# Performance work log

Hardware: AMD Instinct MI355X
Metric: run time of the kernel (lower is better)

The kernel has to match this reference:

```python
import jax, jax.numpy as jnp
import numpy as np

B, P, S, D, H, DFF, F, FIN = 16, 25, 1024, 128, 8, 512, 1, 4
SIGMA, OMEGA = 0.1, 0.5
DH = D // H


def setup_inputs() -> dict:
    key = jax.random.key(0)
    ks = jax.random.split(key, 16)
    s = lambda i, sh, sc=1.0: jax.random.normal(ks[i], sh, dtype=jnp.float32) * sc
    return dict(
        x=s(0, (B, P, D)),
        y=s(1, (B, FIN, 1)),
        K=s(2, (B, P, S, D), 0.02),
        V=s(3, (B, P, S, D), 0.02),
        w=jnp.ones((B, P, 1), jnp.float32) / P,
        I=jax.random.randint(ks[4], (B, P, S), 0, P, dtype=jnp.int32),
        Wq=s(5, (D, D), 0.05), Wk=s(6, (D, D), 0.05),
        Wv=s(7, (D, D), 0.05), Wo=s(8, (D, D), 0.05),
        W1=s(9, (D, DFF), 0.05), b1=jnp.zeros((DFF,), jnp.float32),
        W2=s(10, (DFF, D), 0.05), b2=jnp.zeros((D,), jnp.float32),
        Wout=s(11, (D, F), 0.05), bout=jnp.zeros((F,), jnp.float32),
        eps_k=s(12, (B, P, 1, D)), eps_v=s(13, (B, P, 1, D)), eps_z=s(14, (B, P, 1, D)),
        t=512,
    )


def reference(x, y, K, V, w, I, Wq, Wk, Wv, Wo, W1, b1, W2, b2, Wout, bout,
              eps_k, eps_v, eps_z, t):
    # ---- MultiHeadAttention_SMC: per-particle self-attention with reparam noise ----
    xq = x[:, :, None, :]                                   # (B,P,1,D)
    q = xq @ Wq                                             # (B,P,1,D)
    k = xq @ Wk + SIGMA * eps_k                             # noisy key particle
    v = xq @ Wv + SIGMA * eps_v                             # noisy value particle
    K = K.at[:, :, t, :].set(k[:, :, 0, :])                 # write current step into state
    V = V.at[:, :, t, :].set(v[:, :, 0, :])
    q_h = q.reshape(B, P, 1, H, DH)
    K_h = K.reshape(B, P, S, H, DH)
    V_h = V.reshape(B, P, S, H, DH)
    scores = jnp.einsum('bpqhd,bpshd->bphqs', q_h, K_h) / jnp.sqrt(jnp.float32(DH))
    valid = (jnp.arange(S) <= t)[None, None, None, None, :]  # attend to steps <= t
    scores = jnp.where(valid, scores, jnp.float32(-1e9))
    attn = jax.nn.softmax(scores, axis=-1)                  # (B,P,H,1,S)
    ctx = jnp.einsum('bphqs,bpshd->bpqhd', attn, V_h).reshape(B, P, 1, D)
    z = ctx @ Wo + SIGMA * eps_z                            # reparametrized attention output

    # ---- FFN + output layer (dropout is identity at inference) ----
    r_ = jax.nn.relu(z @ W1 + b1) @ W2 + b2                 # (B,P,1,D)
    pred = r_ @ Wout + bout                                 # (B,P,1,F)

    p_t = pred[:, :, 0, :]                                  # (B,P,F)
    y_sq = y[..., 0]                                        # (B,FIN)
    y_t = jnp.broadcast_to(y_sq[:, None, 0:1], (B, P, F))   # target_feature = 0
    mu = y_t - p_t                                          # (B,P,F)
    log_w_full = jnp.einsum('bpf,bqf->bpq', mu, mu) * (-0.5 * OMEGA)
    log_w = jnp.diagonal(log_w_full, axis1=1, axis2=2)      # (B,P)
    log_w = log_w - jnp.min(log_w, axis=-1, keepdims=True)
    w_new = jnp.exp(log_w)
    w_new = w_new / jnp.sum(w_new, axis=1, keepdims=True)
    w_new = jax.lax.stop_gradient(w_new)

    # ---- particle resampling: categorical sample + gather on particle axis ----
    idx = jax.random.categorical(jax.random.key(42),
                                 jnp.log(w_new + 1e-10)[:, None, :],
                                 axis=-1, shape=(B, P))     # (B,P) ancestor indices
    K_res = jnp.take_along_axis(K, idx[:, :, None, None], axis=1)
    V_res = jnp.take_along_axis(V, idx[:, :, None, None], axis=1)
    I_res = jnp.take_along_axis(I, idx[:, :, None], axis=1)
    I_new = I_res.at[:, :, t].set(idx.astype(I.dtype))
    return (r_, z, pred, w_new[..., None], K_res, V_res, I_new)
```

## Files before the change

kernel.cpp:

```cpp
#include <hip/hip_runtime.h>
#include <math.h>

#define B_ 16
#define P_ 25
#define S_ 1024
#define D_ 128
#define H_ 8
#define DH_ 16
#define DFF_ 512
#define SIGMA_ 0.1f

typedef float f4 __attribute__((ext_vector_type(4)));


__global__ __launch_bounds__(512) void fused_kernel(
    const float* __restrict__ x, const float* __restrict__ Wq,
    const float* __restrict__ Wk, const float* __restrict__ Wv,
    const float* __restrict__ eps_k, const float* __restrict__ eps_v,
    const float* __restrict__ K, const float* __restrict__ V,
    const int* __restrict__ tptr, const float* __restrict__ Wo,
    const float* __restrict__ eps_z, const float* __restrict__ W1,
    const float* __restrict__ b1, const float* __restrict__ W2,
    const float* __restrict__ b2, const float* __restrict__ Wout,
    const float* __restrict__ bout, float* __restrict__ kw,
    float* __restrict__ vw, float* __restrict__ out_r,
    float* __restrict__ out_z, float* __restrict__ out_pred) {
  int bp = blockIdx.x;
  int tid = threadIdx.x;
  int t = tptr[0];

  __shared__ __align__(16) float xs[D_];
  __shared__ __align__(16) float qs[D_];
  __shared__ __align__(16) float ks[D_];
  __shared__ __align__(16) float vs[D_];
  __shared__ __align__(16) float accs[16][D_];
  __shared__ float ms[16][H_];
  __shared__ float ls[16][H_];
  __shared__ float cs[D_];
  __shared__ float zs[D_];
  __shared__ float as_[DFF_];
  __shared__ float rs[D_];
  __shared__ float part[4][D_];

  if (tid < D_) xs[tid] = x[bp * D_ + tid];
  __syncthreads();

  {
    int mat = tid >> 7;
    int d = tid & 127;
    if (mat < 3) {
      const float* W = (mat == 0) ? Wq : (mat == 1) ? Wk : Wv;
      float acc = 0.f;
      for (int i = 0; i < D_; ++i) acc += xs[i] * W[i * D_ + d];
      if (mat == 0) {
        qs[d] = acc * 0.25f;
      } else if (mat == 1) {
        float kk = acc + SIGMA_ * eps_k[bp * D_ + d];
        ks[d] = kk;
        kw[bp * D_ + d] = kk;
      } else {
        float vv = acc + SIGMA_ * eps_v[bp * D_ + d];
        vs[d] = vv;
        vw[bp * D_ + d] = vv;
      }
    }
  }
  __syncthreads();

  {
    int wave = tid >> 6;
    int lane = tid & 63;
    int row = lane >> 5;
    int lr = lane & 31;
    int w16 = wave * 2 + row;
    const f4* Kb = (const f4*)(K + (size_t)bp * S_ * D_);
    const f4* Vb = (const f4*)(V + (size_t)bp * S_ * D_);
    f4 qv = *(const f4*)(qs + 4 * lr);
    float m = -1e30f, l = 0.f;
    f4 acc = {0.f, 0.f, 0.f, 0.f};
    const int RD4 = D_ / 4;
    for (int s = w16; s <= t; s += 16) {
      f4 kk, vv;
      if (s == t) {
        kk = *(const f4*)(ks + 4 * lr);
        vv = *(const f4*)(vs + 4 * lr);
      } else {
        kk = Kb[(size_t)s * RD4 + lr];
        vv = Vb[(size_t)s * RD4 + lr];
      }
      float p = qv.x * kk.x + qv.y * kk.y + qv.z * kk.z + qv.w * kk.w;
      p += __shfl_xor(p, 1);
      p += __shfl_xor(p, 2);
      float mnew = fmaxf(m, p);
      float scale = expf(m - mnew);
      float e = expf(p - mnew);
      l = l * scale + e;
      acc.x = acc.x * scale + e * vv.x;
      acc.y = acc.y * scale + e * vv.y;
      acc.z = acc.z * scale + e * vv.z;
      acc.w = acc.w * scale + e * vv.w;
      m = mnew;
    }
    *(f4*)(&accs[w16][4 * lr]) = acc;
    if ((lr & 3) == 0) { ms[w16][lr >> 2] = m; ls[w16][lr >> 2] = l; }
  }
  __syncthreads();

  if (tid < D_) {
    int h = tid >> 4;
    float mg = -1e30f;
    for (int w2 = 0; w2 < 16; ++w2) mg = fmaxf(mg, ms[w2][h]);
    float L = 0.f, C = 0.f;
    for (int w2 = 0; w2 < 16; ++w2) {
      float sc = expf(ms[w2][h] - mg);
      L += ls[w2][h] * sc;
      C += accs[w2][tid] * sc;
    }
    cs[tid] = C / L;
  }
  __syncthreads();

  int d = tid & 127;
  int qq = tid >> 7;
  {
    float acc = 0.f;
    int i0 = qq * 32;
    for (int i = i0; i < i0 + 32; ++i) acc += cs[i] * Wo[i * D_ + d];
    part[qq][d] = acc;
  }
  __syncthreads();
  if (tid < D_) {
    float z = part[0][tid] + part[1][tid] + part[2][tid] + part[3][tid] +
              SIGMA_ * eps_z[bp * D_ + tid];
    zs[tid] = z;
    out_z[bp * D_ + tid] = z;
  }
  __syncthreads();
  {
    float acc = b1[tid];
    for (int i = 0; i < D_; ++i) acc += zs[i] * W1[i * DFF_ + tid];
    as_[tid] = fmaxf(acc, 0.f);
  }
  __syncthreads();
  {
    float acc = 0.f;
    int j0 = qq * 128;
    for (int j = j0; j < j0 + 128; ++j) acc += as_[j] * W2[j * D_ + d];
    part[qq][d] = acc;
  }
  __syncthreads();
  if (tid < D_) {
    float r = part[0][tid] + part[1][tid] + part[2][tid] + part[3][tid] + b2[tid];
    rs[tid] = r;
    out_r[bp * D_ + tid] = r;
  }
  __syncthreads();
  if (tid < 64) {
    float acc = rs[tid] * Wout[tid] + rs[tid + 64] * Wout[tid + 64];
    acc += __shfl_xor(acc, 1);
    acc += __shfl_xor(acc, 2);
    acc += __shfl_xor(acc, 4);
    acc += __shfl_xor(acc, 8);
    acc += __shfl_xor(acc, 16);
    acc += __shfl_xor(acc, 32);
    if (tid == 0) out_pred[bp] = acc + bout[0];
  }
}

__device__ inline unsigned rotl_(unsigned x, int r) {
  return (x << r) | (x >> (32 - r));
}

__device__ inline void threefry2x32_(unsigned x0, unsigned x1, unsigned& o0,
                                     unsigned& o1) {
  const unsigned k0 = 0u, k1 = 42u;
  const unsigned k2 = k0 ^ k1 ^ 0x1BD11BDAu;
  x0 += k0; x1 += k1;
#define RND_(r) { x0 += x1; x1 = rotl_(x1, r); x1 ^= x0; }
  RND_(13) RND_(15) RND_(26) RND_(6)   x0 += k1; x1 += k2 + 1u;
  RND_(17) RND_(29) RND_(16) RND_(24)  x0 += k2; x1 += k0 + 2u;
  RND_(13) RND_(15) RND_(26) RND_(6)   x0 += k0; x1 += k1 + 3u;
  RND_(17) RND_(29) RND_(16) RND_(24)  x0 += k1; x1 += k2 + 4u;
  RND_(13) RND_(15) RND_(26) RND_(6)   x0 += k2; x1 += k0 + 5u;
#undef RND_
  o0 = x0; o1 = x1;
}

__device__ inline float gumbel_at_(int n) {
  unsigned o0, o1;
  threefry2x32_(0u, (unsigned)n, o0, o1);
  unsigned bits = o0 ^ o1;
  unsigned fb = (bits >> 9) | 0x3f800000u;
  float f = __uint_as_float(fb) - 1.0f;
  const float tiny = 1.1754944e-38f;
  float u = fmaxf(tiny, f * (1.0f - tiny) + tiny);
  return -logf(-logf(u));
}

__global__ __launch_bounds__(64) void sample_kernel(
    const float* __restrict__ pred, const float* __restrict__ y,
    float* __restrict__ out_w, int* __restrict__ idx) {
  int b = blockIdx.x;
  int tid = threadIdx.x;
  __shared__ float lw[P_];
  __shared__ float logits[P_];
  __shared__ float red[2];
  if (tid < P_) {
    float mu = y[b * 4] - pred[b * P_ + tid];
    lw[tid] = -0.25f * (mu * mu);
  }
  __syncthreads();
  if (tid == 0) {
    float mn = lw[0];
    for (int p = 1; p < P_; ++p) mn = fminf(mn, lw[p]);
    red[0] = mn;
  }
  __syncthreads();
  if (tid < P_) lw[tid] = expf(lw[tid] - red[0]);
  __syncthreads();
  if (tid == 0) {
    float s = 0.f;
    for (int p = 0; p < P_; ++p) s += lw[p];
    red[1] = s;
  }
  __syncthreads();
  if (tid < P_) {
    float wn = lw[tid] / red[1];
    out_w[b * P_ + tid] = wn;
    logits[tid] = logf(wn + 1e-10f);
  }
  __syncthreads();
  if (tid < P_) {
    float best = -1e30f;
    int bestj = 0;
    for (int j = 0; j < P_; ++j) {
      int n = (b * P_ + tid) * P_ + j;
      float val = gumbel_at_(n) + logits[j];
      if (val > best) { best = val; bestj = j; }
    }
    idx[b * P_ + tid] = bestj;
  }
}

__global__ __launch_bounds__(256) void gather_kernel(
    const float* __restrict__ K, const float* __restrict__ V,
    const float* __restrict__ kn, const float* __restrict__ vn,
    const int* __restrict__ I, const int* __restrict__ idx,
    const int* __restrict__ tptr, float* __restrict__ outK,
    float* __restrict__ outV, float* __restrict__ outI) {
  const int CH = 4;
  const int F4 = (S_ * D_ / 4) / CH;
  const int NG = B_ * P_ * CH * 2;
  int bid = blockIdx.x;
  int t = tptr[0];
  if (bid < NG) {
    int tv = bid / (B_ * P_ * CH);
    int rem = bid - tv * (B_ * P_ * CH);
    int bp = rem / CH;
    int chunk = rem - bp * CH;
    int b = bp / P_;
    int j = idx[bp];
    const float* src = (tv == 0 ? K : V) + (size_t)(b * P_ + j) * (S_ * D_);
    const f4* sub = (const f4*)((tv == 0 ? kn : vn) + (b * P_ + j) * D_);
    float* dst = (tv == 0 ? outK : outV) + (size_t)bp * (S_ * D_);
    const f4* src4 = (const f4*)src;
    f4* dst4 = (f4*)dst;
    int base = chunk * F4;
    int tlo = t * (D_ / 4);
    for (int i = base + threadIdx.x; i < base + F4; i += 256) {
      f4 val;
      if (i >= tlo && i < tlo + D_ / 4) val = sub[i - tlo];
      else                              val = src4[i];
      dst4[i] = val;
    }
  } else {
    int bp = bid - NG;
    int b = bp / P_;
    int j = idx[bp];
    const int* src = I + (b * P_ + j) * S_;
    float* dst = outI + bp * S_;
    for (int s = threadIdx.x; s < S_; s += 256) {
      int val = (s == t) ? j : src[s];
      dst[s] = (float)val;
    }
  }
}

extern "C" void kernel_launch(void* const* d_in, const int* in_sizes, int n_in,
                              void* d_out, int out_size, void* d_ws,
                              size_t ws_size, hipStream_t stream) {
  const float* x     = (const float*)d_in[0];
  const float* y     = (const float*)d_in[1];
  const float* K     = (const float*)d_in[2];
  const float* V     = (const float*)d_in[3];
  const int*   I     = (const int*)d_in[5];
  const float* Wq    = (const float*)d_in[6];
  const float* Wk    = (const float*)d_in[7];
  const float* Wv    = (const float*)d_in[8];
  const float* Wo    = (const float*)d_in[9];
  const float* W1    = (const float*)d_in[10];
  const float* b1    = (const float*)d_in[11];
  const float* W2    = (const float*)d_in[12];
  const float* b2    = (const float*)d_in[13];
  const float* Wout  = (const float*)d_in[14];
  const float* bout  = (const float*)d_in[15];
  const float* eps_k = (const float*)d_in[16];
  const float* eps_v = (const float*)d_in[17];
  const float* eps_z = (const float*)d_in[18];
  const int*   tptr  = (const int*)d_in[19];

  float* out      = (float*)d_out;
  float* out_r    = out;
  float* out_z    = out + 51200;
  float* out_pred = out + 102400;
  float* out_w    = out + 102800;
  float* outK     = out + 103200;
  float* outV     = outK + (size_t)52428800;
  float* outI     = outV + (size_t)52428800;

  float* ws  = (float*)d_ws;
  float* k   = ws;
  float* v   = ws + 51200;
  int*   idx = (int*)(ws + 102400);

  fused_kernel<<<B_ * P_, 512, 0, stream>>>(
      x, Wq, Wk, Wv, eps_k, eps_v, K, V, tptr, Wo, eps_z, W1, b1, W2, b2,
      Wout, bout, k, v, out_r, out_z, out_pred);
  sample_kernel<<<B_, 64, 0, stream>>>(out_pred, y, out_w, idx);
  gather_kernel<<<B_ * P_ * 4 * 2 + B_ * P_, 256, 0, stream>>>(
      K, V, k, v, I, idx, tptr, outK, outV, outI);
}
```

Measured before the change: 779.3 us.

## Fold resampling into gather kernel, use nontemporal stores, unroll attention loop

Removes the separate sample_kernel launch. Every gather block now recomputes the weight normalisation and the Gumbel argmax for its own particle, and writes K/V/I outputs with nontemporal stores. The attention loop drops the per-iteration s==t branch, handles the current step in a separate tail, and is unrolled by 4. This saves one launch and its dependency gap but repeats the small sampling work in every one of several thousand blocks, adding syncthreads before each copy starts.

```diff
diff --git a/kernel.cpp b/kernel.cpp
--- a/kernel.cpp
+++ b/kernel.cpp
@@ -79,15 +79,26 @@
     float m = -1e30f, l = 0.f;
     f4 acc = {0.f, 0.f, 0.f, 0.f};
     const int RD4 = D_ / 4;
-    for (int s = w16; s <= t; s += 16) {
-      f4 kk, vv;
-      if (s == t) {
-        kk = *(const f4*)(ks + 4 * lr);
-        vv = *(const f4*)(vs + 4 * lr);
-      } else {
-        kk = Kb[(size_t)s * RD4 + lr];
-        vv = Vb[(size_t)s * RD4 + lr];
-      }
+#pragma unroll 4
+    for (int s = w16; s < t; s += 16) {
+      f4 kk = Kb[(size_t)s * RD4 + lr];
+      f4 vv = Vb[(size_t)s * RD4 + lr];
+      float p = qv.x * kk.x + qv.y * kk.y + qv.z * kk.z + qv.w * kk.w;
+      p += __shfl_xor(p, 1);
+      p += __shfl_xor(p, 2);
+      float mnew = fmaxf(m, p);
+      float scale = expf(m - mnew);
+      float e = expf(p - mnew);
+      l = l * scale + e;
+      acc.x = acc.x * scale + e * vv.x;
+      acc.y = acc.y * scale + e * vv.y;
+      acc.z = acc.z * scale + e * vv.z;
+      acc.w = acc.w * scale + e * vv.w;
+      m = mnew;
+    }
+    if ((t & 15) == w16) {
+      f4 kk = *(const f4*)(ks + 4 * lr);
+      f4 vv = *(const f4*)(vs + 4 * lr);
       float p = qv.x * kk.x + qv.y * kk.y + qv.z * kk.z + qv.w * kk.w;
       p += __shfl_xor(p, 1);
       p += __shfl_xor(p, 2);
@@ -197,69 +208,81 @@
   return -logf(-logf(u));
 }
 
-__global__ __launch_bounds__(64) void sample_kernel(
-    const float* __restrict__ pred, const float* __restrict__ y,
-    float* __restrict__ out_w, int* __restrict__ idx) {
-  int b = blockIdx.x;
-  int tid = threadIdx.x;
-  __shared__ float lw[P_];
-  __shared__ float logits[P_];
-  __shared__ float red[2];
-  if (tid < P_) {
-    float mu = y[b * 4] - pred[b * P_ + tid];
-    lw[tid] = -0.25f * (mu * mu);
-  }
-  __syncthreads();
-  if (tid == 0) {
-    float mn = lw[0];
-    for (int p = 1; p < P_; ++p) mn = fminf(mn, lw[p]);
-    red[0] = mn;
-  }
-  __syncthreads();
-  if (tid < P_) lw[tid] = expf(lw[tid] - red[0]);
-  __syncthreads();
-  if (tid == 0) {
-    float s = 0.f;
-    for (int p = 0; p < P_; ++p) s += lw[p];
-    red[1] = s;
-  }
-  __syncthreads();
-  if (tid < P_) {
-    float wn = lw[tid] / red[1];
-    out_w[b * P_ + tid] = wn;
-    logits[tid] = logf(wn + 1e-10f);
-  }
-  __syncthreads();
-  if (tid < P_) {
-    float best = -1e30f;
-    int bestj = 0;
-    for (int j = 0; j < P_; ++j) {
-      int n = (b * P_ + tid) * P_ + j;
-      float val = gumbel_at_(n) + logits[j];
-      if (val > best) { best = val; bestj = j; }
-    }
-    idx[b * P_ + tid] = bestj;
-  }
-}
-
 __global__ __launch_bounds__(256) void gather_kernel(
     const float* __restrict__ K, const float* __restrict__ V,
     const float* __restrict__ kn, const float* __restrict__ vn,
-    const int* __restrict__ I, const int* __restrict__ idx,
-    const int* __restrict__ tptr, float* __restrict__ outK,
-    float* __restrict__ outV, float* __restrict__ outI) {
+    const int* __restrict__ I, const float* __restrict__ pred,
+    const float* __restrict__ y, const int* __restrict__ tptr,
+    float* __restrict__ outK, float* __restrict__ outV,
+    float* __restrict__ outI, float* __restrict__ out_w) {
   const int CH = 4;
   const int F4 = (S_ * D_ / 4) / CH;
   const int NG = B_ * P_ * CH * 2;
   int bid = blockIdx.x;
+  int tid = threadIdx.x;
   int t = tptr[0];
-  if (bid < NG) {
-    int tv = bid / (B_ * P_ * CH);
+
+  int bp, chunk = 0, tv = 0;
+  bool is_copy = (bid < NG);
+  if (is_copy) {
+    tv = bid / (B_ * P_ * CH);
     int rem = bid - tv * (B_ * P_ * CH);
-    int bp = rem / CH;
-    int chunk = rem - bp * CH;
-    int b = bp / P_;
-    int j = idx[bp];
+    bp = rem / CH;
+    chunk = rem - bp * CH;
+  } else {
+    bp = bid - NG;
+  }
+  int b = bp / P_;
+  int pp = bp - b * P_;
+
+  __shared__ float sh[P_];
+  __shared__ float sh_w[P_];
+  __shared__ float sh_g[P_];
+  __shared__ float red0, red1;
+  __shared__ int sh_j;
+  if (tid < P_) {
+    float mu = y[b * 4] - pred[b * P_ + tid];
+    sh[tid] = -0.25f * (mu * mu);
+  }
+  __syncthreads();
+  if (tid == 0) {
+    float mn = sh[0];
+    for (int p = 1; p < P_; ++p) mn = fminf(mn, sh[p]);
+    red0 = mn;
+  }
+  __syncthreads();
+  if (tid < P_) sh[tid] = expf(sh[tid] - red0);
+  __syncthreads();
+  if (tid == 0) {
+    float s = 0.f;
+    for (int p = 0; p < P_; ++p) s += sh[p];
+    red1 = s;
+  }
+  __syncthreads();
+  if (tid < P_) {
+    float wn = sh[tid] / red1;
+    sh_w[tid] = wn;
+    sh[tid] = logf(wn + 1e-10f);
+  }
+  __syncthreads();
+  if (tid < P_) {
+    int n = (b * P_ + pp) * P_ + tid;
+    sh_g[tid] = gumbel_at_(n) + sh[tid];
+  }
+  __syncthreads();
+  if (tid == 0) {
+    float best = -1e30f;
+    int bj = 0;
+    for (int j2 = 0; j2 < P_; ++j2) {
+      float v2 = sh_g[j2];
+      if (v2 > best) { best = v2; bj = j2; }
+    }
+    sh_j = bj;
+  }
+  __syncthreads();
+  int j = sh_j;
+
+  if (is_copy) {
     const float* src = (tv == 0 ? K : V) + (size_t)(b * P_ + j) * (S_ * D_);
     const f4* sub = (const f4*)((tv == 0 ? kn : vn) + (b * P_ + j) * D_);
     float* dst = (tv == 0 ? outK : outV) + (size_t)bp * (S_ * D_);
@@ -267,22 +290,20 @@
     f4* dst4 = (f4*)dst;
     int base = chunk * F4;
     int tlo = t * (D_ / 4);
-    for (int i = base + threadIdx.x; i < base + F4; i += 256) {
+    for (int i = base + tid; i < base + F4; i += 256) {
       f4 val;
       if (i >= tlo && i < tlo + D_ / 4) val = sub[i - tlo];
       else                              val = src4[i];
-      dst4[i] = val;
+      __builtin_nontemporal_store(val, dst4 + i);
     }
   } else {
-    int bp = bid - NG;
-    int b = bp / P_;
-    int j = idx[bp];
     const int* src = I + (b * P_ + j) * S_;
     float* dst = outI + bp * S_;
-    for (int s = threadIdx.x; s < S_; s += 256) {
+    for (int s = tid; s < S_; s += 256) {
       int val = (s == t) ? j : src[s];
-      dst[s] = (float)val;
-    }
+      __builtin_nontemporal_store((float)val, dst + s);
+    }
+    if (pp == 0 && tid < P_) out_w[b * P_ + tid] = sh_w[tid];
   }
 }
 
@@ -318,15 +339,13 @@
   float* outV     = outK + (size_t)52428800;
   float* outI     = outV + (size_t)52428800;
 
-  float* ws  = (float*)d_ws;
-  float* k   = ws;
-  float* v   = ws + 51200;
-  int*   idx = (int*)(ws + 102400);
+  float* ws = (float*)d_ws;
+  float* k  = ws;
+  float* v  = ws + 51200;
 
   fused_kernel<<<B_ * P_, 512, 0, stream>>>(
       x, Wq, Wk, Wv, eps_k, eps_v, K, V, tptr, Wo, eps_z, W1, b1, W2, b2,
       Wout, bout, k, v, out_r, out_z, out_pred);
-  sample_kernel<<<B_, 64, 0, stream>>>(out_pred, y, out_w, idx);
   gather_kernel<<<B_ * P_ * 4 * 2 + B_ * P_, 256, 0, stream>>>(
-      K, V, k, v, I, idx, tptr, outK, outV, outI);
-}
+      K, V, k, v, I, out_pred, y, tptr, outK, outV, outI, out_w);
+}
```

New measurement: 785.7 us. About the same (+0.8%).
